# Performance work log

Hardware: AMD Instinct MI355X
Metric: run time of the kernel (lower is better)

The kernel has to match this reference:

```python
import jax, jax.numpy as jnp
import numpy as np

E = 128; H = 8; DK = 16; FFH = 512; NL = 6
DEPOT = 20; CUST = 500; N = DEPOT + CUST
B = 32; M = N; L = 40; CLIP = 10.0; EPS = 1e-5


def _heads(x):
    b, n, _ = x.shape
    return x.reshape(b, n, H, DK).transpose(0, 2, 1, 3)  # (b,H,n,dk)


def _mha(q, k, v, mask3=None):
    s = jnp.einsum('bhnd,bhmd->bhnm', q, k) / jnp.sqrt(jnp.float32(DK))
    if mask3 is not None:
        s = s + mask3[:, None, :, :]
    w = jax.nn.softmax(s, axis=-1)
    o = jnp.einsum('bhnm,bhmd->bhnd', w, v)
    return o.transpose(0, 2, 1, 3).reshape(q.shape[0], q.shape[2], H * DK)


def _inorm(x, g, b):  # InstanceNorm1d over the node axis, per (batch, channel)
    mu = x.mean(axis=1, keepdims=True)
    var = x.var(axis=1, keepdims=True)
    return (x - mu) / jnp.sqrt(var + EPS) * g + b


def setup_inputs() -> dict:
    key = jax.random.key(0)
    ks = jax.random.split(key, 30)
    rn = lambda k, s, sc=0.05: (jax.random.normal(k, s, dtype=jnp.float32) * sc)
    inp = {
        'depot_feats': jax.random.normal(ks[0], (B, DEPOT, 4), dtype=jnp.float32),
        'customer_feats': jax.random.normal(ks[1], (B, CUST, 3), dtype=jnp.float32),
        'mask': jnp.zeros((B, M, N), dtype=jnp.float32),
        'load': jax.random.uniform(ks[2], (B, M), dtype=jnp.float32),
        'current_node': jax.random.randint(ks[3], (B, M), 0, N),
        'subtour_nodes': jax.random.randint(ks[4], (B, M, L), 0, N),
        'subtour_len': jax.random.randint(ks[5], (B, M), 0, L),
        'selected': jax.random.randint(ks[6], (B, M, 4), 0, N),
        # encoder embedding layers
        'enc_dep_W': rn(ks[7], (E, 4)), 'enc_dep_b': rn(ks[8], (E,)),
        'enc_cus_W': rn(ks[9], (E, 3)), 'enc_cus_b': rn(ks[10], (E,)),
        # stacked encoder-layer params
        'Wq': rn(ks[11], (NL, E, E)), 'Wk': rn(ks[12], (NL, E, E)),
        'Wv': rn(ks[13], (NL, E, E)),
        'Wc': rn(ks[14], (NL, E, E)), 'Wc_b': rn(ks[15], (NL, E)),
        'n1_g': jnp.ones((NL, E), jnp.float32), 'n1_b': jnp.zeros((NL, E), jnp.float32),
        'ffW1': rn(ks[16], (NL, FFH, E)), 'ffb1': rn(ks[17], (NL, FFH)),
        'ffW2': rn(ks[18], (NL, E, FFH)), 'ffb2': rn(ks[19], (NL, E)),
        'n2_g': jnp.ones((NL, E), jnp.float32), 'n2_b': jnp.zeros((NL, E), jnp.float32),
        # decoder params
        'dec_Wq_loc': rn(ks[20], (E, 2 * E)),
        'dec_Wq_rout': rn(ks[21], (E, 2 * E + 1)),
        'dec_Wk': rn(ks[22], (E, E)), 'dec_Wv': rn(ks[23], (E, E)),
        'dec_Wc': rn(ks[24], (E, E)), 'dec_Wc_b': rn(ks[25], (E,)),
    }
    return inp


def reference(depot_feats, customer_feats, mask, load,
              enc_dep_W, enc_dep_b, enc_cus_W, enc_cus_b,
              Wq, Wk, Wv, Wc, Wc_b, n1_g, n1_b,
              ffW1, ffb1, ffW2, ffb2, n2_g, n2_b,
              dec_Wq_loc, dec_Wq_rout, dec_Wk, dec_Wv, dec_Wc, dec_Wc_b,
              current_node, subtour_nodes, subtour_len, selected):
    # ---- Encoder ----
    dep = depot_feats @ enc_dep_W.T + enc_dep_b
    cus = customer_feats @ enc_cus_W.T + enc_cus_b
    x = jnp.concatenate([dep, cus], axis=1)  # (B,N,E)
    for i in range(NL):
        q = _heads(x @ Wq[i].T); k = _heads(x @ Wk[i].T); v = _heads(x @ Wv[i].T)
        mh = _mha(q, k, v) @ Wc[i].T + Wc_b[i]
        x1 = _inorm(x + mh, n1_g[i], n1_b[i])
        ff = jax.nn.relu(x1 @ ffW1[i].T + ffb1[i]) @ ffW2[i].T + ffb2[i]
        x = _inorm(x1 + ff, n2_g[i], n2_b[i])
    encoded = x  # (B,N,E)

    # ---- set_k_v ----
    k_d = _heads(encoded @ dec_Wk.T)
    v_d = _heads(encoded @ dec_Wv.T)

    # ---- Decoder forward (current_node present, last_hh not None branch) ----
    enc_mean = encoded.mean(axis=1, keepdims=True)  # (B,1,E)
    enc_mean = jnp.broadcast_to(enc_mean, (B, M, E))
    b_idx = jnp.arange(B)[:, None]
    last_emb = encoded[b_idx, current_node]  # (B,M,E) gather of current node
    input_cat = jnp.concatenate([last_emb, enc_mean, load[:, :, None]], axis=2)
    q_routing = input_cat @ dec_Wq_rout.T  # (B,M,E)

    # subtour gather + masked mean pool
    bb = jnp.arange(B)[:, None, None]
    sub_embs = encoded[bb, subtour_nodes]  # (B,M,L,E)
    pos = jnp.arange(L)[None, None, :]
    valid = pos < subtour_len[:, :, None]
    is_cust = subtour_nodes >= DEPOT
    fm = (valid & is_cust).astype(jnp.float32)  # (B,M,L)
    sub_sum = jnp.einsum('bmle,bml->bme', sub_embs, fm)
    cnt = jnp.clip(fm.sum(axis=2, keepdims=True), 1.0, None)
    sub_mean = sub_sum / cnt
    q_location = jnp.concatenate([last_emb, sub_mean], axis=2) @ dec_Wq_loc.T

    # conditional query blend
    last_node = selected[:, :, -2] < DEPOT
    node = current_node < DEPOT
    flag = ((~last_node) & node).astype(jnp.float32)[:, :, None]  # (B,M,1)
    final_q = q_location * flag + q_routing * (1.0 - flag)

    q = _heads(final_q)  # (B,H,M,dk)
    attn = _mha(q, k_d, v_d, mask3=mask)  # (B,M,H*dk)
    score = attn @ dec_Wc.T + dec_Wc_b  # (B,M,E)
    score_nodes = jnp.einsum('bme,bne->bmn', score, encoded)
    score_scaled = score_nodes / jnp.sqrt(jnp.float32(E))
    score_masked = CLIP * jnp.tanh(score_scaled) + mask
    prob = jax.nn.softmax(score_masked, axis=2)
    return prob
```

## Files before the change

### kernel.cpp

```cpp
#include <hip/hip_runtime.h>
#include <hip/hip_bf16.h>

#define BB 32
#define NN 520
#define MM 520
#define EE 128
#define HH 8
#define DKK 16
#define FFH_ 512
#define NL_ 6
#define DEPOT_ 20
#define LL 40

typedef short short8 __attribute__((ext_vector_type(8)));
typedef short bshort4 __attribute__((ext_vector_type(4)));
typedef float floatx4 __attribute__((ext_vector_type(4)));

__device__ __forceinline__ unsigned short f2b(float x) {
    unsigned int u = __float_as_uint(x);
    return (unsigned short)((u + 0x7fffu + ((u >> 16) & 1u)) >> 16);
}
__device__ __forceinline__ unsigned short f2b_t(float x) {
    return (unsigned short)(__float_as_uint(x) >> 16);
}
__device__ __forceinline__ float b2f_(unsigned short h) {
    return __uint_as_float(((unsigned int)h) << 16);
}

__global__ __launch_bounds__(256) void embed_k(
    const float* __restrict__ dep, const float* __restrict__ cus,
    const float* __restrict__ Wd, const float* __restrict__ bd,
    const float* __restrict__ Wc3, const float* __restrict__ bc,
    float* __restrict__ x)
{
    int idx = blockIdx.x * 256 + threadIdx.x;
    int e = idx & 127;
    int bn = idx >> 7;
    int n = bn % NN;
    int b = bn / NN;
    float a;
    if (n < DEPOT_) {
        a = bd[e];
        const float* f = dep + ((size_t)(b * DEPOT_ + n)) * 4;
        #pragma unroll
        for (int j = 0; j < 4; j++) a += f[j] * Wd[e * 4 + j];
    } else {
        a = bc[e];
        const float* f = cus + ((size_t)(b * 500 + (n - DEPOT_))) * 3;
        #pragma unroll
        for (int j = 0; j < 3; j++) a += f[j] * Wc3[e * 3 + j];
    }
    x[idx] = a;
}

#define WLS 196608
#define WDEC 1179648
#define WTOT 1277952
__global__ __launch_bounds__(256) void wconv_k(
    const float* __restrict__ Wq, const float* __restrict__ Wk, const float* __restrict__ Wv,
    const float* __restrict__ Wc, const float* __restrict__ fW1, const float* __restrict__ fW2,
    const float* __restrict__ dWk, const float* __restrict__ dWv, const float* __restrict__ dWc,
    const float* __restrict__ Wql, const float* __restrict__ Wqr,
    unsigned short* __restrict__ WH, unsigned short* __restrict__ WL)
{
    int idx = blockIdx.x * 256 + threadIdx.x;
    if (idx >= WTOT) return;
    const float* src;
    if (idx < WDEC) {
        int i = idx / WLS, r = idx % WLS;
        if (r < 49152) {
            int row = r >> 7, col = r & 127;
            const float* w = row < 128 ? Wq : (row < 256 ? Wk : Wv);
            src = w + (size_t)i * 16384 + (size_t)(row & 127) * 128 + col;
        } else if (r < 65536) {
            src = Wc + (size_t)i * 16384 + (r - 49152);
        } else if (r < 131072) {
            src = fW1 + (size_t)i * 65536 + (r - 65536);
        } else {
            src = fW2 + (size_t)i * 65536 + (r - 131072);
        }
    } else {
        int r = idx - WDEC;
        if (r < 32768) {
            int row = r >> 7, col = r & 127;
            src = (row < 128 ? dWk : dWv) + (size_t)(row & 127) * 128 + col;
        } else if (r < 49152) {
            src = dWc + (r - 32768);
        } else {
            int rr = r - 49152;
            int row = rr >> 7, col = rr & 127;
            if (row < 128)      src = Wqr + (size_t)row * 257 + col;
            else if (row < 256) src = Wql + (size_t)(row - 128) * 256 + col;
            else                src = Wql + (size_t)(row - 256) * 256 + 128 + col;
        }
    }
    float v = *src;
    unsigned short h = f2b(v);
    WH[idx] = h;
    WL[idx] = f2b(v - b2f_(h));
}

#define AP 40
__global__ __launch_bounds__(256) void gemm_pc_k(
    const float* __restrict__ A, int lda,
    const unsigned short* __restrict__ WH, const unsigned short* __restrict__ WL, int ldw,
    const float* __restrict__ bias,
    float* __restrict__ C, int ldc,
    int K, int relu)
{
    __shared__ __align__(16) unsigned short Ah[2][64][AP];
    __shared__ __align__(16) unsigned short Al[2][64][AP];
    __shared__ __align__(16) unsigned short Bh[2][64][AP];
    __shared__ __align__(16) unsigned short Bl[2][64][AP];

    int t = threadIdx.x;
    int w = t >> 6, lane = t & 63;
    int frow = lane & 15, fq = lane >> 4;
    int n0 = blockIdx.x * 64, m0 = blockIdx.y * 64;

    int arow = t & 63, acol = (t >> 6) * 8;

    const float* Abase = A + (size_t)(m0 + arow) * lda + acol;
    const unsigned short* WHb = WH + (size_t)(n0 + arow) * ldw + acol;
    const unsigned short* WLb = WL + (size_t)(n0 + arow) * ldw + acol;

    floatx4 acc[4];
    #pragma unroll
    for (int j = 0; j < 4; j++) acc[j] = (floatx4){0.0f, 0.0f, 0.0f, 0.0f};

    {
        float4 v0 = ((const float4*)Abase)[0];
        float4 v1 = ((const float4*)Abase)[1];
        float vr[8] = {v0.x, v0.y, v0.z, v0.w, v1.x, v1.y, v1.z, v1.w};
        short8 hv, lv;
        #pragma unroll
        for (int j = 0; j < 8; j++) {
            unsigned short h = f2b(vr[j]);
            hv[j] = (short)h;
            lv[j] = (short)f2b(vr[j] - b2f_(h));
        }
        *((short8*)&Ah[0][arow][acol]) = hv;
        *((short8*)&Al[0][arow][acol]) = lv;
        *((short8*)&Bh[0][arow][acol]) = *((const short8*)WHb);
        *((short8*)&Bl[0][arow][acol]) = *((const short8*)WLb);
    }
    __syncthreads();

    int nkt = K >> 5;
    for (int kt = 0; kt < nkt; kt++) {
        int cur = kt & 1;
        bool pf = (kt + 1 < nkt);

        float4 av0, av1;
        short8 nbh, nbl;
        if (pf) {
            const float* Ap = Abase + (kt + 1) * 32;
            av0 = ((const float4*)Ap)[0];
            av1 = ((const float4*)Ap)[1];
            nbh = *((const short8*)(WHb + (kt + 1) * 32));
            nbl = *((const short8*)(WLb + (kt + 1) * 32));
        }

        short8 ah = *((const short8*)&Ah[cur][w * 16 + frow][fq * 8]);
        short8 al = *((const short8*)&Al[cur][w * 16 + frow][fq * 8]);
        #pragma unroll
        for (int nt = 0; nt < 4; nt++) {
            short8 bh = *((const short8*)&Bh[cur][nt * 16 + frow][fq * 8]);
            short8 bl = *((const short8*)&Bl[cur][nt * 16 + frow][fq * 8]);
            acc[nt] = __builtin_amdgcn_mfma_f32_16x16x32_bf16(ah, bh, acc[nt], 0, 0, 0);
            acc[nt] = __builtin_amdgcn_mfma_f32_16x16x32_bf16(ah, bl, acc[nt], 0, 0, 0);
            acc[nt] = __builtin_amdgcn_mfma_f32_16x16x32_bf16(al, bh, acc[nt], 0, 0, 0);
        }

        if (pf) {
            int nb2 = cur ^ 1;
            float vr[8] = {av0.x, av0.y, av0.z, av0.w, av1.x, av1.y, av1.z, av1.w};
            short8 hv, lv;
            #pragma unroll
            for (int j = 0; j < 8; j++) {
                unsigned short h = f2b(vr[j]);
                hv[j] = (short)h;
                lv[j] = (short)f2b(vr[j] - b2f_(h));
            }
            *((short8*)&Ah[nb2][arow][acol]) = hv;
            *((short8*)&Al[nb2][arow][acol]) = lv;
            *((short8*)&Bh[nb2][arow][acol]) = nbh;
            *((short8*)&Bl[nb2][arow][acol]) = nbl;
        }
        __syncthreads();
    }

    #pragma unroll
    for (int nt = 0; nt < 4; nt++) {
        int col = n0 + nt * 16 + frow;
        float bv = bias ? bias[col] : 0.0f;
        int rbase = m0 + w * 16 + fq * 4;
        #pragma unroll
        for (int r = 0; r < 4; r++) {
            float v = acc[nt][r] + bv;
            if (relu) v = fmaxf(v, 0.0f);
            C[(size_t)(rbase + r) * ldc + col] = v;
        }
    }
}

__global__ __launch_bounds__(256) void gemm_qkv3_k(
    const float* __restrict__ A, int lda,
    const unsigned short* __restrict__ WH, const unsigned short* __restrict__ WL, int ldw,
    float* __restrict__ C0, float* __restrict__ C1, float* __restrict__ C2,
    int ldc, int K, int pack)
{
    __shared__ __align__(16) unsigned short Ah[2][64][AP];
    __shared__ __align__(16) unsigned short Al[2][64][AP];
    __shared__ __align__(16) unsigned short Bh[2][64][AP];
    __shared__ __align__(16) unsigned short Bl[2][64][AP];

    int t = threadIdx.x;
    int w = t >> 6, lane = t & 63;
    int frow = lane & 15, fq = lane >> 4;
    int nb = blockIdx.x;
    int which = nb >> 1;
    float* C = which == 0 ? C0 : (which == 1 ? C1 : C2);
    int n0w = nb * 64;
    int n0c = (nb & 1) * 64;
    int m0 = blockIdx.y * 64;

    int arow = t & 63, acol = (t >> 6) * 8;

    const float* Abase = A + (size_t)(m0 + arow) * lda + acol;
    const unsigned short* WHb = WH + (size_t)(n0w + arow) * ldw + acol;
    const unsigned short* WLb = WL + (size_t)(n0w + arow) * ldw + acol;

    floatx4 acc[4];
    #pragma unroll
    for (int j = 0; j < 4; j++) acc[j] = (floatx4){0.0f, 0.0f, 0.0f, 0.0f};

    {
        float4 v0 = ((const float4*)Abase)[0];
        float4 v1 = ((const float4*)Abase)[1];
        float vr[8] = {v0.x, v0.y, v0.z, v0.w, v1.x, v1.y, v1.z, v1.w};
        short8 hv, lv;
        #pragma unroll
        for (int j = 0; j < 8; j++) {
            unsigned short h = f2b(vr[j]);
            hv[j] = (short)h;
            lv[j] = (short)f2b(vr[j] - b2f_(h));
        }
        *((short8*)&Ah[0][arow][acol]) = hv;
        *((short8*)&Al[0][arow][acol]) = lv;
        *((short8*)&Bh[0][arow][acol]) = *((const short8*)WHb);
        *((short8*)&Bl[0][arow][acol]) = *((const short8*)WLb);
    }
    __syncthreads();

    int nkt = K >> 5;
    for (int kt = 0; kt < nkt; kt++) {
        int cur = kt & 1;
        bool pf = (kt + 1 < nkt);

        float4 av0, av1;
        short8 nbh, nbl;
        if (pf) {
            const float* Ap = Abase + (kt + 1) * 32;
            av0 = ((const float4*)Ap)[0];
            av1 = ((const float4*)Ap)[1];
            nbh = *((const short8*)(WHb + (kt + 1) * 32));
            nbl = *((const short8*)(WLb + (kt + 1) * 32));
        }

        short8 ah = *((const short8*)&Ah[cur][w * 16 + frow][fq * 8]);
        short8 al = *((const short8*)&Al[cur][w * 16 + frow][fq * 8]);
        #pragma unroll
        for (int nt = 0; nt < 4; nt++) {
            short8 bh = *((const short8*)&Bh[cur][nt * 16 + frow][fq * 8]);
            short8 bl = *((const short8*)&Bl[cur][nt * 16 + frow][fq * 8]);
            acc[nt] = __builtin_amdgcn_mfma_f32_16x16x32_bf16(ah, bh, acc[nt], 0, 0, 0);
            acc[nt] = __builtin_amdgcn_mfma_f32_16x16x32_bf16(ah, bl, acc[nt], 0, 0, 0);
            acc[nt] = __builtin_amdgcn_mfma_f32_16x16x32_bf16(al, bh, acc[nt], 0, 0, 0);
        }

        if (pf) {
            int nb2 = cur ^ 1;
            float vr[8] = {av0.x, av0.y, av0.z, av0.w, av1.x, av1.y, av1.z, av1.w};
            short8 hv, lv;
            #pragma unroll
            for (int j = 0; j < 8; j++) {
                unsigned short h = f2b(vr[j]);
                hv[j] = (short)h;
                lv[j] = (short)f2b(vr[j] - b2f_(h));
            }
            *((short8*)&Ah[nb2][arow][acol]) = hv;
            *((short8*)&Al[nb2][arow][acol]) = lv;
            *((short8*)&Bh[nb2][arow][acol]) = nbh;
            *((short8*)&Bl[nb2][arow][acol]) = nbl;
        }
        __syncthreads();
    }

    #pragma unroll
    for (int nt = 0; nt < 4; nt++) {
        int col = n0c + nt * 16 + frow;
        int hh = col >> 4, dd = col & 15;
        int rbase = m0 + w * 16 + fq * 4;
        #pragma unroll
        for (int r = 0; r < 4; r++) {
            int row = rbase + r;
            if (pack) {
                int b2 = row / NN, n2 = row - b2 * NN;
                C[((size_t)(b2 * HH + hh) * NN + n2) * 16 + dd] = acc[nt][r];
            } else {
                C[(size_t)row * ldc + col] = acc[nt][r];
            }
        }
    }
}

#define GT 64
#define GK 32
#define GP 36
__global__ __launch_bounds__(256) void sgemm_k(
    const float* __restrict__ A,
    const float* __restrict__ Enc,
    float* __restrict__ C)
{
    __shared__ float As[GT][GP];
    __shared__ float Ws[GT][GP];
    int t = threadIdx.x;
    int tx = t & 15, ty = t >> 4;
    int b = blockIdx.z;
    int m0 = blockIdx.y * GT, n0 = blockIdx.x * GT;
    int lr = t >> 2, lc = (t & 3) * 8;
    int mr = m0 + lr; if (mr >= NN) mr = NN - 1;
    int nr = n0 + lr; if (nr >= NN) nr = NN - 1;
    float acc[4][4];
    #pragma unroll
    for (int i = 0; i < 4; i++)
        #pragma unroll
        for (int j = 0; j < 4; j++) acc[i][j] = 0.0f;

    for (int k0 = 0; k0 < EE; k0 += GK) {
        const float* Ap = A + ((size_t)(b * NN + mr)) * EE + k0 + lc;
        const float* Wp = Enc + ((size_t)(b * NN + nr)) * EE + k0 + lc;
        float4 av0 = *((const float4*)Ap), av1 = *((const float4*)(Ap + 4));
        float4 wv0 = *((const float4*)Wp), wv1 = *((const float4*)(Wp + 4));
        *((float4*)&As[lr][lc]) = av0; *((float4*)&As[lr][lc + 4]) = av1;
        *((float4*)&Ws[lr][lc]) = wv0; *((float4*)&Ws[lr][lc + 4]) = wv1;
        __syncthreads();
        #pragma unroll
        for (int kk = 0; kk < GK; kk += 2) {
            float2 a0 = *((const float2*)&As[ty][kk]);
            float2 a1 = *((const float2*)&As[ty + 16][kk]);
            float2 a2 = *((const float2*)&As[ty + 32][kk]);
            float2 a3 = *((const float2*)&As[ty + 48][kk]);
            float2 w0 = *((const float2*)&Ws[tx][kk]);
            float2 w1 = *((const float2*)&Ws[tx + 16][kk]);
            float2 w2 = *((const float2*)&Ws[tx + 32][kk]);
            float2 w3 = *((const float2*)&Ws[tx + 48][kk]);
            acc[0][0] += a0.x * w0.x + a0.y * w0.y;
            acc[0][1] += a0.x * w1.x + a0.y * w1.y;
            acc[0][2] += a0.x * w2.x + a0.y * w2.y;
            acc[0][3] += a0.x * w3.x + a0.y * w3.y;
            acc[1][0] += a1.x * w0.x + a1.y * w0.y;
            acc[1][1] += a1.x * w1.x + a1.y * w1.y;
            acc[1][2] += a1.x * w2.x + a1.y * w2.y;
            acc[1][3] += a1.x * w3.x + a1.y * w3.y;
            acc[2][0] += a2.x * w0.x + a2.y * w0.y;
            acc[2][1] += a2.x * w1.x + a2.y * w1.y;
            acc[2][2] += a2.x * w2.x + a2.y * w2.y;
            acc[2][3] += a2.x * w3.x + a2.y * w3.y;
            acc[3][0] += a3.x * w0.x + a3.y * w0.y;
            acc[3][1] += a3.x * w1.x + a3.y * w1.y;
            acc[3][2] += a3.x * w2.x + a3.y * w2.y;
            acc[3][3] += a3.x * w3.x + a3.y * w3.y;
        }
        __syncthreads();
    }
    #pragma unroll
    for (int i = 0; i < 4; i++) {
        int m = m0 + ty + 16 * i;
        if (m >= NN) continue;
        #pragma unroll
        for (int j = 0; j < 4; j++) {
            int n = n0 + tx + 16 * j;
            if (n >= NN) continue;
            float v = 10.0f * tanhf(acc[i][j] * 0.088388347648318447f);
            C[((size_t)(b * NN + m)) * NN + n] = v;
        }
    }
}

__global__ __launch_bounds__(64) void smax_k(
    const float* __restrict__ L, const float* __restrict__ mask,
    float* __restrict__ out)
{
    int bm = blockIdx.x;
    int t = threadIdx.x;
    const float* Lr = L + (size_t)bm * NN;
    const float* Mr = mask + (size_t)bm * NN;
    float v[9];
    float mx = -1e30f;
    #pragma unroll
    for (int i = 0; i < 9; i++) {
        int idx = t + i * 64;
        if (idx < NN) { v[i] = Lr[idx] + Mr[idx]; mx = fmaxf(mx, v[i]); }
        else v[i] = -1e30f;
    }
    #pragma unroll
    for (int o = 32; o > 0; o >>= 1) mx = fmaxf(mx, __shfl_xor(mx, o));
    float s = 0.0f;
    #pragma unroll
    for (int i = 0; i < 9; i++) {
        int idx = t + i * 64;
        float e = (idx < NN) ? expf(v[i] - mx) : 0.0f;
        v[i] = e; s += e;
    }
    #pragma unroll
    for (int o = 32; o > 0; o >>= 1) s += __shfl_xor(s, o);
    float inv = 1.0f / s;
    #pragma unroll
    for (int i = 0; i < 9; i++) {
        int idx = t + i * 64;
        if (idx < NN) out[(size_t)bm * NN + idx] = v[i] * inv;
    }
}

#define ATK 64
#define NFRG 3
__global__ __launch_bounds__(256) void fmha_pers_k(
    const float* __restrict__ Qp, const float* __restrict__ Kp,
    const float* __restrict__ Vp, const float* __restrict__ mask,
    float* __restrict__ O, int Nq, int Nk)
{
    __shared__ __align__(16) unsigned short Khl[2][ATK][40];
    __shared__ __align__(16) unsigned short Vhi[2][16][72];
    __shared__ __align__(16) unsigned short Vlo[2][16][72];

    int b = blockIdx.x, h = blockIdx.y, z = blockIdx.z;
    int bh = b * HH + h;
    int t = threadIdx.x;
    int w = t >> 6, lane = t & 63;
    int r16 = lane & 15, g = lane >> 4;

    short8 qf[NFRG], qs[NFRG];
    floatx4 o_acc[NFRG];
    float m_i[NFRG], l_i[NFRG];
    const float* mrowf[NFRG];
    const float* QpB = Qp + (size_t)bh * Nq * 16;
    #pragma unroll
    for (int f = 0; f < NFRG; f++) {
        int fi = f * 16 + z * 4 + w;
        int qg = fi * 16 + r16;
        int qc = qg < Nq ? qg : Nq - 1;
        const float* qp = QpB + (size_t)qc * 16 + 8 * (g & 1);
        float4 qv0 = *((const float4*)qp);
        float4 qv1 = *((const float4*)(qp + 4));
        float qa[8] = {qv0.x, qv0.y, qv0.z, qv0.w, qv1.x, qv1.y, qv1.z, qv1.w};
        #pragma unroll
        for (int j = 0; j < 8; j++) {
            unsigned short hh = f2b_t(qa[j]);
            unsigned short ll = f2b_t(qa[j] - b2f_(hh));
            qf[f][j] = (short)(g < 2 ? hh : ll);
            qs[f][j] = (short)(g < 2 ? ll : hh);
        }
        o_acc[f] = (floatx4){0.0f, 0.0f, 0.0f, 0.0f};
        m_i[f] = -1e30f; l_i[f] = 0.0f;
        mrowf[f] = mask ? (mask + ((size_t)(b * Nq + qc)) * Nk) : nullptr;
    }

    int srow = t >> 2, sc = (t & 3) * 4;
    const float* KpB = Kp + ((size_t)bh * Nk) * 16 + sc;
    const float* VpB = Vp + ((size_t)bh * Nk) * 16 + sc;

    {
        int krc = srow < Nk ? srow : Nk - 1;
        float4 kv = *((const float4*)(KpB + (size_t)krc * 16));
        float4 vv = *((const float4*)(VpB + (size_t)krc * 16));
        float ka[4] = {kv.x, kv.y, kv.z, kv.w};
        float va[4] = {vv.x, vv.y, vv.z, vv.w};
        bshort4 khv, klv;
        #pragma unroll
        for (int j = 0; j < 4; j++) {
            unsigned short hh = f2b_t(ka[j]);
            khv[j] = (short)hh;
            klv[j] = (short)f2b_t(ka[j] - b2f_(hh));
        }
        *((bshort4*)&Khl[0][srow][sc])      = khv;
        *((bshort4*)&Khl[0][srow][16 + sc]) = klv;
        #pragma unroll
        for (int j = 0; j < 4; j++) {
            unsigned short hh = f2b_t(va[j]);
            Vhi[0][sc + j][srow] = hh;
            Vlo[0][sc + j][srow] = f2b_t(va[j] - b2f_(hh));
        }
    }
    __syncthreads();

    int nkt = (Nk + ATK - 1) / ATK;
    for (int kt = 0; kt < nkt; kt++) {
        int cur = kt & 1;
        int k0 = kt * ATK;

        float4 nkv, nvv;
        bool pf = (kt + 1 < nkt);
        if (pf) {
            int kr = k0 + ATK + srow;
            int krc = kr < Nk ? kr : Nk - 1;
            nkv = *((const float4*)(KpB + (size_t)krc * 16));
            nvv = *((const float4*)(VpB + (size_t)krc * 16));
        }

        short8 kfr[4];
        bshort4 vhf[4], vlf[4];
        #pragma unroll
        for (int s = 0; s < 4; s++) {
            kfr[s] = *((const short8*)&Khl[cur][s * 16 + r16][8 * g]);
            vhf[s] = *((const bshort4*)&Vhi[cur][r16][s * 16 + 4 * g]);
            vlf[s] = *((const bshort4*)&Vlo[cur][r16][s * 16 + 4 * g]);
        }

        #pragma unroll
        for (int f = 0; f < NFRG; f++) {
            int fi = f * 16 + z * 4 + w;
            if (fi * 16 >= Nq) continue;

            float mv[4][4];
            if (mask) {
                #pragma unroll
                for (int s = 0; s < 4; s++) {
                    int c0 = k0 + s * 16 + 4 * g;
                    if (c0 + 3 < Nk) {
                        float4 m4 = *((const float4*)(mrowf[f] + c0));
                        mv[s][0] = m4.x; mv[s][1] = m4.y;
                        mv[s][2] = m4.z; mv[s][3] = m4.w;
                    } else {
                        #pragma unroll
                        for (int r = 0; r < 4; r++)
                            mv[s][r] = (c0 + r < Nk) ? mrowf[f][c0 + r] : 0.0f;
                    }
                }
            }

            float p[4][4];
            #pragma unroll
            for (int s = 0; s < 4; s++) {
                floatx4 a = (floatx4){0.0f, 0.0f, 0.0f, 0.0f};
                a = __builtin_amdgcn_mfma_f32_16x16x32_bf16(kfr[s], qf[f], a, 0, 0, 0);
                a = __builtin_amdgcn_mfma_f32_16x16x32_bf16(kfr[s], qs[f], a, 0, 0, 0);
                #pragma unroll
                for (int r = 0; r < 4; r++) p[s][r] = a[r];
            }

            #pragma unroll
            for (int s = 0; s < 4; s++) {
                int c0 = k0 + s * 16 + 4 * g;
                #pragma unroll
                for (int r = 0; r < 4; r++) {
                    float mvr = mask ? mv[s][r] : 0.0f;
                    p[s][r] = (c0 + r < Nk) ? (p[s][r] * 0.25f + mvr) : -1e30f;
                }
            }

            float tmax = -1e30f;
            #pragma unroll
            for (int s = 0; s < 4; s++)
                #pragma unroll
                for (int r = 0; r < 4; r++) tmax = fmaxf(tmax, p[s][r]);
            tmax = fmaxf(tmax, __shfl_xor(tmax, 16));
            tmax = fmaxf(tmax, __shfl_xor(tmax, 32));
            float m_new = fmaxf(m_i[f], tmax);
            float alpha = __expf(m_i[f] - m_new);
            float lloc = 0.0f;
            #pragma unroll
            for (int s = 0; s < 4; s++) {
                #pragma unroll
                for (int r = 0; r < 4; r++) {
                    float e = __expf(p[s][r] - m_new);
                    p[s][r] = e; lloc += e;
                }
            }
            lloc += __shfl_xor(lloc, 16);
            lloc += __shfl_xor(lloc, 32);
            l_i[f] = l_i[f] * alpha + lloc;
            m_i[f] = m_new;
            #pragma unroll
            for (int r = 0; r < 4; r++) {
                float ar = __shfl(alpha, 4 * g + r);
                o_acc[f][r] *= ar;
            }

            #pragma unroll
            for (int s = 0; s < 4; s++) {
                bshort4 ph, pl;
                #pragma unroll
                for (int r = 0; r < 4; r++) {
                    unsigned short hh = f2b_t(p[s][r]);
                    ph[r] = (short)hh;
                    pl[r] = (short)f2b_t(p[s][r] - b2f_(hh));
                }
                o_acc[f] = __builtin_amdgcn_mfma_f32_16x16x16bf16_1k(ph, vhf[s], o_acc[f], 0, 0, 0);
                o_acc[f] = __builtin_amdgcn_mfma_f32_16x16x16bf16_1k(ph, vlf[s], o_acc[f], 0, 0, 0);
                o_acc[f] = __builtin_amdgcn_mfma_f32_16x16x16bf16_1k(pl, vhf[s], o_acc[f], 0, 0, 0);
            }
        }

        if (pf) {
            int nb2 = cur ^ 1;
            float ka[4] = {nkv.x, nkv.y, nkv.z, nkv.w};
            float va[4] = {nvv.x, nvv.y, nvv.z, nvv.w};
            bshort4 khv, klv;
            #pragma unroll
            for (int j = 0; j < 4; j++) {
                unsigned short hh = f2b_t(ka[j]);
                khv[j] = (short)hh;
                klv[j] = (short)f2b_t(ka[j] - b2f_(hh));
            }
            *((bshort4*)&Khl[nb2][srow][sc])      = khv;
            *((bshort4*)&Khl[nb2][srow][16 + sc]) = klv;
            #pragma unroll
            for (int j = 0; j < 4; j++) {
                unsigned short hh = f2b_t(va[j]);
                Vhi[nb2][sc + j][srow] = hh;
                Vlo[nb2][sc + j][srow] = f2b_t(va[j] - b2f_(hh));
            }
        }
        __syncthreads();
    }

    #pragma unroll
    for (int f = 0; f < NFRG; f++) {
        int fi = f * 16 + z * 4 + w;
        if (fi * 16 >= Nq) continue;
        #pragma unroll
        for (int r = 0; r < 4; r++) {
            float lr = __shfl(l_i[f], 4 * g + r);
            int qrow = fi * 16 + 4 * g + r;
            if (qrow < Nq)
                O[((size_t)(b * Nq + qrow)) * EE + h * 16 + r16] = o_acc[f][r] / lr;
        }
    }
}

__global__ __launch_bounds__(256) void inorm_k(
    const float* __restrict__ X, const float* __restrict__ Y,
    const float* __restrict__ g, const float* __restrict__ bb,
    float* __restrict__ Out)
{
    int b = blockIdx.x, eg = blockIdx.y;
    int t = threadIdx.x;
    int tx = t & 15, tn = t >> 4;
    int e = eg * 16 + tx;
    const float* Xb = X + ((size_t)b * NN) * EE + e;
    const float* Yb = Y + ((size_t)b * NN) * EE + e;
    float s = 0.0f, s2 = 0.0f;
    for (int n = tn; n < NN; n += 16) {
        float v = Xb[(size_t)n * EE] + Yb[(size_t)n * EE];
        s += v; s2 += v * v;
    }
    __shared__ float rs[16][17], rs2[16][17];
    rs[tn][tx] = s; rs2[tn][tx] = s2;
    __syncthreads();
    float st = 0.0f, st2 = 0.0f;
    #pragma unroll
    for (int j = 0; j < 16; j++) { st += rs[j][tx]; st2 += rs2[j][tx]; }
    float mu = st * (1.0f / NN);
    float var = st2 * (1.0f / NN) - mu * mu;
    float inv = rsqrtf(var + 1e-5f);
    float gg = g[e], bv = bb[e];
    float* Ob = Out + ((size_t)b * NN) * EE + e;
    for (int n = tn; n < NN; n += 16) {
        float v = Xb[(size_t)n * EE] + Yb[(size_t)n * EE];
        Ob[(size_t)n * EE] = (v - mu) * inv * gg + bv;
    }
}

__global__ void zero_k(float* p, int n) {
    int i = blockIdx.x * 256 + threadIdx.x;
    if (i < n) p[i] = 0.0f;
}

__global__ __launch_bounds__(128) void encsum_k(const float* __restrict__ enc, float* __restrict__ esum) {
    int b = blockIdx.x, ch = blockIdx.y, t = threadIdx.x;
    float a = 0.0f;
    for (int i = 0; i < 65; i++) {
        int n = ch * 65 + i;
        a += enc[((size_t)(b * NN + n)) * EE + t];
    }
    atomicAdd(&esum[b * EE + t], a);
}

__global__ __launch_bounds__(128) void meanterm_k(
    const float* __restrict__ esum, const float* __restrict__ Wr, float* __restrict__ mt)
{
    int b = blockIdx.x, t = threadIdx.x;
    __shared__ float em[128];
    em[t] = esum[b * EE + t] * (1.0f / NN);
    __syncthreads();
    const float* w = Wr + (size_t)t * 257 + 128;
    float a = 0.0f;
    for (int f = 0; f < 128; f++) a += em[f] * w[f];
    mt[b * EE + t] = a;
}

__global__ __launch_bounds__(128) void subtour_k(
    const float* __restrict__ enc, const int* __restrict__ subn,
    const int* __restrict__ subl, float* __restrict__ subm)
{
    int bm = blockIdx.x;
    int b = bm / MM;
    int t = threadIdx.x;
    int len = subl[bm];
    float acc = 0.0f; int cnt = 0;
    for (int l = 0; l < LL; l++) {
        int node = subn[(size_t)bm * LL + l];
        if (l < len && node >= DEPOT_) {
            acc += enc[((size_t)(b * NN + node)) * EE + t];
            cnt++;
        }
    }
    float cf = (float)(cnt < 1 ? 1 : cnt);
    subm[(size_t)bm * EE + t] = acc / cf;
}

__global__ __launch_bounds__(128) void decq_gather_k(
    const float* __restrict__ R, const float* __restrict__ L1, const float* __restrict__ SM2,
    const float* __restrict__ mterm, const int* __restrict__ cur,
    const float* __restrict__ loadv, const int* __restrict__ sel,
    const float* __restrict__ Wqr, float* __restrict__ out)
{
    int bm = blockIdx.x;
    int b = bm / MM;
    int m = bm - b * MM;
    int t = threadIdx.x;
    int cn = cur[bm];
    int s2v = sel[(size_t)bm * 4 + 2];
    bool flag = (s2v >= DEPOT_) && (cn < DEPOT_);
    size_t eo = ((size_t)(b * NN + cn)) * EE + t;
    float q;
    if (flag) q = L1[eo] + SM2[(size_t)bm * EE + t];
    else      q = R[eo] + mterm[b * EE + t] + loadv[bm] * Wqr[(size_t)t * 257 + 256];
    out[((size_t)(b * HH + (t >> 4)) * MM + m) * 16 + (t & 15)] = q;
}

extern "C" void kernel_launch(void* const* d_in, const int* in_sizes, int n_in,
                              void* d_out, int out_size, void* d_ws, size_t ws_size,
                              hipStream_t stream)
{
    const float* depot = (const float*)d_in[0];
    const float* cust  = (const float*)d_in[1];
    const float* mask  = (const float*)d_in[2];
    const float* loadv = (const float*)d_in[3];
    const int*  cur   = (const int*)d_in[4];
    const int*  subn  = (const int*)d_in[5];
    const int*  subl  = (const int*)d_in[6];
    const int*  sel   = (const int*)d_in[7];
    const float* Wdep  = (const float*)d_in[8];
    const float* bdep  = (const float*)d_in[9];
    const float* Wcus  = (const float*)d_in[10];
    const float* bcus  = (const float*)d_in[11];
    const float* Wq    = (const float*)d_in[12];
    const float* Wk    = (const float*)d_in[13];
    const float* Wv    = (const float*)d_in[14];
    const float* Wc    = (const float*)d_in[15];
    const float* Wcb   = (const float*)d_in[16];
    const float* n1g   = (const float*)d_in[17];
    const float* n1b   = (const float*)d_in[18];
    const float* fW1   = (const float*)d_in[19];
    const float* fb1   = (const float*)d_in[20];
    const float* fW2   = (const float*)d_in[21];
    const float* fb2   = (const float*)d_in[22];
    const float* n2g   = (const float*)d_in[23];
    const float* n2b   = (const float*)d_in[24];
    const float* Wql   = (const float*)d_in[25];
    const float* Wqr   = (const float*)d_in[26];
    const float* dWk   = (const float*)d_in[27];
    const float* dWv   = (const float*)d_in[28];
    const float* dWc   = (const float*)d_in[29];
    const float* dWcb  = (const float*)d_in[30];

    const size_t SZ = (size_t)BB * NN * EE;
    float* f0 = (float*)d_ws;
    float* f1 = f0 + SZ;
    float* f2 = f1 + SZ;
    float* f3 = f2 + SZ;
    float* f4 = f3 + SZ;
    float* f5 = f4 + SZ;
    float* big = f5 + SZ;
    unsigned short* WHp = (unsigned short*)(big + (size_t)BB * NN * FFH_);
    unsigned short* WLp = WHp + WTOT;

    dim3 g4(EE / 64, (BB * NN) / 64);
    dim3 g16(FFH_ / 64, (BB * NN) / 64);
    dim3 gq3(6, (BB * NN) / 64);
    dim3 gq2(4, (BB * NN) / 64);
    dim3 gmha(BB, HH, 4);
    dim3 gin(BB, 8);
    dim3 gsc((NN + GT - 1) / GT, (NN + GT - 1) / GT, BB);

    wconv_k<<<(WTOT + 255) / 256, 256, 0, stream>>>(Wq, Wk, Wv, Wc, fW1, fW2,
                                                    dWk, dWv, dWc, Wql, Wqr, WHp, WLp);
    embed_k<<<(BB * NN * EE) / 256, 256, 0, stream>>>(depot, cust, Wdep, bdep, Wcus, bcus, f0);

    for (int i = 0; i < NL_; i++) {
        const unsigned short* lH = WHp + (size_t)i * WLS;
        const unsigned short* lL = WLp + (size_t)i * WLS;
        gemm_qkv3_k<<<gq3, 256, 0, stream>>>(f0, EE, lH, lL, EE, f1, f2, f3, EE, EE, 1);
        fmha_pers_k<<<gmha, 256, 0, stream>>>(f1, f2, f3, nullptr, f4, NN, NN);
        gemm_pc_k<<<g4, 256, 0, stream>>>(f4, EE, lH + 49152, lL + 49152, EE, Wcb + i * EE, f1, EE, EE, 0);
        inorm_k<<<gin, 256, 0, stream>>>(f0, f1, n1g + i * EE, n1b + i * EE, f5);
        gemm_pc_k<<<g16, 256, 0, stream>>>(f5, EE, lH + 65536, lL + 65536, EE, fb1 + i * FFH_, big, FFH_, EE, 1);
        gemm_pc_k<<<g4, 256, 0, stream>>>(big, FFH_, lH + 131072, lL + 131072, FFH_, fb2 + i * EE, f1, EE, FFH_, 0);
        inorm_k<<<gin, 256, 0, stream>>>(f5, f1, n2g + i * EE, n2b + i * EE, f0);
    }

    const unsigned short* dH = WHp + WDEC;
    const unsigned short* dL = WLp + WDEC;
    gemm_qkv3_k<<<gq2, 256, 0, stream>>>(f0, EE, dH, dL, EE, f1, f2, f2, EE, EE, 1);

    zero_k<<<(BB * EE + 255) / 256, 256, 0, stream>>>(f3, BB * EE);
    encsum_k<<<dim3(BB, 8), 128, 0, stream>>>(f0, f3);
    meanterm_k<<<BB, 128, 0, stream>>>(f3, Wqr, f3 + BB * EE);
    subtour_k<<<BB * MM, 128, 0, stream>>>(f0, subn, subl, f4);

    gemm_qkv3_k<<<gq2, 256, 0, stream>>>(f0, EE, dH + 49152, dL + 49152, EE, big, big + SZ, big + SZ, EE, EE, 0);
    gemm_pc_k<<<g4, 256, 0, stream>>>(f4, EE, dH + 49152 + 32768, dL + 49152 + 32768, EE, nullptr, big + 2 * SZ, EE, EE, 0);
    decq_gather_k<<<BB * MM, 128, 0, stream>>>(big, big + SZ, big + 2 * SZ, f3 + BB * EE, cur, loadv, sel, Wqr, f5);

    fmha_pers_k<<<gmha, 256, 0, stream>>>(f5, f1, f2, mask, f4, MM, NN);
    gemm_pc_k<<<g4, 256, 0, stream>>>(f4, EE, dH + 32768, dL + 32768, EE, dWcb, big, EE, EE, 0);

    sgemm_k<<<gsc, 256, 0, stream>>>(big, f0, f1);
    smax_k<<<BB * MM, 64, 0, stream>>>(f1, mask, (float*)d_out);
}
```

Baseline: 1.474 ms.

## Use split-bf16 MFMA for decoder score GEMM and hoist mask loads in attention

Replaces the scalar FP32 shared-memory GEMM that computes decoder scores against encoder outputs with a double-buffered MFMA kernel. Operands are split into bf16 hi/lo pairs and combined with three MFMAs to keep near-fp32 accuracy. Separately, in the flash-attention kernel, mask values for all query fragments are loaded before the K/V fragment reads, so global mask latency can overlap the LDS loads. This raises register pressure and adds conversion work, and the split-bf16 path drops the lo*lo term, so results may differ slightly from fp32.

```diff
diff --git a/kernel.cpp b/kernel.cpp
--- a/kernel.cpp
+++ b/kernel.cpp
@@ -315,75 +315,113 @@
     }
 }
 
-#define GT 64
-#define GK 32
-#define GP 36
 __global__ __launch_bounds__(256) void sgemm_k(
     const float* __restrict__ A,
     const float* __restrict__ Enc,
     float* __restrict__ C)
 {
-    __shared__ float As[GT][GP];
-    __shared__ float Ws[GT][GP];
+    __shared__ __align__(16) unsigned short Ah[2][64][AP];
+    __shared__ __align__(16) unsigned short Al[2][64][AP];
+    __shared__ __align__(16) unsigned short Bh[2][64][AP];
+    __shared__ __align__(16) unsigned short Bl[2][64][AP];
+
     int t = threadIdx.x;
-    int tx = t & 15, ty = t >> 4;
+    int w = t >> 6, lane = t & 63;
+    int frow = lane & 15, fq = lane >> 4;
     int b = blockIdx.z;
-    int m0 = blockIdx.y * GT, n0 = blockIdx.x * GT;
-    int lr = t >> 2, lc = (t & 3) * 8;
-    int mr = m0 + lr; if (mr >= NN) mr = NN - 1;
-    int nr = n0 + lr; if (nr >= NN) nr = NN - 1;
-    float acc[4][4];
-    #pragma unroll
-    for (int i = 0; i < 4; i++)
-        #pragma unroll
-        for (int j = 0; j < 4; j++) acc[i][j] = 0.0f;
-
-    for (int k0 = 0; k0 < EE; k0 += GK) {
-        const float* Ap = A + ((size_t)(b * NN + mr)) * EE + k0 + lc;
-        const float* Wp = Enc + ((size_t)(b * NN + nr)) * EE + k0 + lc;
-        float4 av0 = *((const float4*)Ap), av1 = *((const float4*)(Ap + 4));
-        float4 wv0 = *((const float4*)Wp), wv1 = *((const float4*)(Wp + 4));
-        *((float4*)&As[lr][lc]) = av0; *((float4*)&As[lr][lc + 4]) = av1;
-        *((float4*)&Ws[lr][lc]) = wv0; *((float4*)&Ws[lr][lc + 4]) = wv1;
+    int n0 = blockIdx.x * 64, m0 = blockIdx.y * 64;
+
+    int arow = t & 63, acol = (t >> 6) * 8;
+    int mr = m0 + arow; if (mr >= NN) mr = NN - 1;
+    int nr = n0 + arow; if (nr >= NN) nr = NN - 1;
+
+    const float* Abase = A + ((size_t)(b * NN + mr)) * EE + acol;
+    const float* Bbase = Enc + ((size_t)(b * NN + nr)) * EE + acol;
+
+    floatx4 acc[4];
+    #pragma unroll
+    for (int j = 0; j < 4; j++) acc[j] = (floatx4){0.0f, 0.0f, 0.0f, 0.0f};
+
+    {
+        float4 a0 = ((const float4*)Abase)[0];
+        float4 a1 = ((const float4*)Abase)[1];
+        float4 b0 = ((const float4*)Bbase)[0];
+        float4 b1 = ((const float4*)Bbase)[1];
+        float ar[8] = {a0.x, a0.y, a0.z, a0.w, a1.x, a1.y, a1.z, a1.w};
+        float br[8] = {b0.x, b0.y, b0.z, b0.w, b1.x, b1.y, b1.z, b1.w};
+        short8 ahv, alv, bhv, blv;
+        #pragma unroll
+        for (int j = 0; j < 8; j++) {
+            unsigned short h = f2b_t(ar[j]);
+            ahv[j] = (short)h;
+            alv[j] = (short)f2b_t(ar[j] - b2f_(h));
+            unsigned short g2 = f2b_t(br[j]);
+            bhv[j] = (short)g2;
+            blv[j] = (short)f2b_t(br[j] - b2f_(g2));
+        }
+        *((short8*)&Ah[0][arow][acol]) = ahv;
+        *((short8*)&Al[0][arow][acol]) = alv;
+        *((short8*)&Bh[0][arow][acol]) = bhv;
+        *((short8*)&Bl[0][arow][acol]) = blv;
+    }
+    __syncthreads();
+
+    int nkt = EE >> 5;
+    for (int kt = 0; kt < nkt; kt++) {
+        int cur = kt & 1;
+        bool pf = (kt + 1 < nkt);
+
+        float4 a0, a1, b0, b1;
+        if (pf) {
+            const float* Ap = Abase + (kt + 1) * 32;
+            const float* Bp = Bbase + (kt + 1) * 32;
+            a0 = ((const float4*)Ap)[0]; a1 = ((const float4*)Ap)[1];
+            b0 = ((const float4*)Bp)[0]; b1 = ((const float4*)Bp)[1];
+        }
+
+        short8 ah = *((const short8*)&Ah[cur][w * 16 + frow][fq * 8]);
+        short8 al = *((const short8*)&Al[cur][w * 16 + frow][fq * 8]);
+        #pragma unroll
+        for (int nt = 0; nt < 4; nt++) {
+            short8 bh = *((const short8*)&Bh[cur][nt * 16 + frow][fq * 8]);
+            short8 bl = *((const short8*)&Bl[cur][nt * 16 + frow][fq * 8]);
+            acc[nt] = __builtin_amdgcn_mfma_f32_16x16x32_bf16(ah, bh, acc[nt], 0, 0, 0);
+            acc[nt] = __builtin_amdgcn_mfma_f32_16x16x32_bf16(ah, bl, acc[nt], 0, 0, 0);
+            acc[nt] = __builtin_amdgcn_mfma_f32_16x16x32_bf16(al, bh, acc[nt], 0, 0, 0);
+        }
+
+        if (pf) {
+            int nb2 = cur ^ 1;
+            float ar[8] = {a0.x, a0.y, a0.z, a0.w, a1.x, a1.y, a1.z, a1.w};
+            float br[8] = {b0.x, b0.y, b0.z, b0.w, b1.x, b1.y, b1.z, b1.w};
+            short8 ahv, alv, bhv, blv;
+            #pragma unroll
+            for (int j = 0; j < 8; j++) {
+                unsigned short h = f2b_t(ar[j]);
+                ahv[j] = (short)h;
+                alv[j] = (short)f2b_t(ar[j] - b2f_(h));
+                unsigned short g2 = f2b_t(br[j]);
+                bhv[j] = (short)g2;
+                blv[j] = (short)f2b_t(br[j] - b2f_(g2));
+            }
+            *((short8*)&Ah[nb2][arow][acol]) = ahv;
+            *((short8*)&Al[nb2][arow][acol]) = alv;
+            *((short8*)&Bh[nb2][arow][acol]) = bhv;
+            *((short8*)&Bl[nb2][arow][acol]) = blv;
+        }
         __syncthreads();
-        #pragma unroll
-        for (int kk = 0; kk < GK; kk += 2) {
-            float2 a0 = *((const float2*)&As[ty][kk]);
-            float2 a1 = *((const float2*)&As[ty + 16][kk]);
-            float2 a2 = *((const float2*)&As[ty + 32][kk]);
-            float2 a3 = *((const float2*)&As[ty + 48][kk]);
-            float2 w0 = *((const float2*)&Ws[tx][kk]);
-            float2 w1 = *((const float2*)&Ws[tx + 16][kk]);
-            float2 w2 = *((const float2*)&Ws[tx + 32][kk]);
-            float2 w3 = *((const float2*)&Ws[tx + 48][kk]);
-            acc[0][0] += a0.x * w0.x + a0.y * w0.y;
-            acc[0][1] += a0.x * w1.x + a0.y * w1.y;
-            acc[0][2] += a0.x * w2.x + a0.y * w2.y;
-            acc[0][3] += a0.x * w3.x + a0.y * w3.y;
-            acc[1][0] += a1.x * w0.x + a1.y * w0.y;
-            acc[1][1] += a1.x * w1.x + a1.y * w1.y;
-            acc[1][2] += a1.x * w2.x + a1.y * w2.y;
-            acc[1][3] += a1.x * w3.x + a1.y * w3.y;
-            acc[2][0] += a2.x * w0.x + a2.y * w0.y;
-            acc[2][1] += a2.x * w1.x + a2.y * w1.y;
-            acc[2][2] += a2.x * w2.x + a2.y * w2.y;
-            acc[2][3] += a2.x * w3.x + a2.y * w3.y;
-            acc[3][0] += a3.x * w0.x + a3.y * w0.y;
-            acc[3][1] += a3.x * w1.x + a3.y * w1.y;
-            acc[3][2] += a3.x * w2.x + a3.y * w2.y;
-            acc[3][3] += a3.x * w3.x + a3.y * w3.y;
-        }
-        __syncthreads();
-    }
-    #pragma unroll
-    for (int i = 0; i < 4; i++) {
-        int m = m0 + ty + 16 * i;
-        if (m >= NN) continue;
-        #pragma unroll
-        for (int j = 0; j < 4; j++) {
-            int n = n0 + tx + 16 * j;
-            if (n >= NN) continue;
-            float v = 10.0f * tanhf(acc[i][j] * 0.088388347648318447f);
+    }
+
+    #pragma unroll
+    for (int nt = 0; nt < 4; nt++) {
+        int n = n0 + nt * 16 + frow;
+        if (n >= NN) continue;
+        int rbase = m0 + w * 16 + fq * 4;
+        #pragma unroll
+        for (int r = 0; r < 4; r++) {
+            int m = rbase + r;
+            if (m >= NN) continue;
+            float v = 10.0f * tanhf(acc[nt][r] * 0.088388347648318447f);
             C[((size_t)(b * NN + m)) * NN + n] = v;
         }
     }
@@ -509,36 +547,39 @@
             nvv = *((const float4*)(VpB + (size_t)krc * 16));
         }
 
-        short8 kfr[4];
-        bshort4 vhf[4], vlf[4];
-        #pragma unroll
-        for (int s = 0; s < 4; s++) {
-            kfr[s] = *((const short8*)&Khl[cur][s * 16 + r16][8 * g]);
-            vhf[s] = *((const bshort4*)&Vhi[cur][r16][s * 16 + 4 * g]);
-            vlf[s] = *((const bshort4*)&Vlo[cur][r16][s * 16 + 4 * g]);
-        }
-
-        #pragma unroll
-        for (int f = 0; f < NFRG; f++) {
-            int fi = f * 16 + z * 4 + w;
-            if (fi * 16 >= Nq) continue;
-
-            float mv[4][4];
-            if (mask) {
+        float mvv[NFRG][4][4];
+        if (mask) {
+            #pragma unroll
+            for (int f = 0; f < NFRG; f++) {
                 #pragma unroll
                 for (int s = 0; s < 4; s++) {
                     int c0 = k0 + s * 16 + 4 * g;
                     if (c0 + 3 < Nk) {
                         float4 m4 = *((const float4*)(mrowf[f] + c0));
-                        mv[s][0] = m4.x; mv[s][1] = m4.y;
-                        mv[s][2] = m4.z; mv[s][3] = m4.w;
+                        mvv[f][s][0] = m4.x; mvv[f][s][1] = m4.y;
+                        mvv[f][s][2] = m4.z; mvv[f][s][3] = m4.w;
                     } else {
                         #pragma unroll
                         for (int r = 0; r < 4; r++)
-                            mv[s][r] = (c0 + r < Nk) ? mrowf[f][c0 + r] : 0.0f;
+                            mvv[f][s][r] = (c0 + r < Nk) ? mrowf[f][c0 + r] : 0.0f;
                     }
                 }
             }
+        }
+
+        short8 kfr[4];
+        bshort4 vhf[4], vlf[4];
+        #pragma unroll
+        for (int s = 0; s < 4; s++) {
+            kfr[s] = *((const short8*)&Khl[cur][s * 16 + r16][8 * g]);
+            vhf[s] = *((const bshort4*)&Vhi[cur][r16][s * 16 + 4 * g]);
+            vlf[s] = *((const bshort4*)&Vlo[cur][r16][s * 16 + 4 * g]);
+        }
+
+        #pragma unroll
+        for (int f = 0; f < NFRG; f++) {
+            int fi = f * 16 + z * 4 + w;
+            if (fi * 16 >= Nq) continue;
 
             float p[4][4];
             #pragma unroll
@@ -555,8 +596,8 @@
                 int c0 = k0 + s * 16 + 4 * g;
                 #pragma unroll
                 for (int r = 0; r < 4; r++) {
-                    float mvr = mask ? mv[s][r] : 0.0f;
-                    p[s][r] = (c0 + r < Nk) ? (p[s][r] * 0.25f + mvr) : -1e30f;
+                    float mv = mask ? mvv[f][s][r] : 0.0f;
+                    p[s][r] = (c0 + r < Nk) ? (p[s][r] * 0.25f + mv) : -1e30f;
                 }
             }
 
@@ -794,7 +835,7 @@
     dim3 gq2(4, (BB * NN) / 64);
     dim3 gmha(BB, HH, 4);
     dim3 gin(BB, 8);
-    dim3 gsc((NN + GT - 1) / GT, (NN + GT - 1) / GT, BB);
+    dim3 gsc((NN + 63) / 64, (NN + 63) / 64, BB);
 
     wconv_k<<<(WTOT + 255) / 256, 256, 0, stream>>>(Wq, Wk, Wv, Wc, fW1, fW2,
                                                     dWk, dWv, dWc, Wql, Wqr, WHp, WLp);
```

After: 1.441 ms. 1.02x faster.
